# Kernel optimization log

Measured on AMD Instinct MI355X. Metric: run time of the kernel, lower is better.

The kernel has to match this reference:

```python
import jax, jax.numpy as jnp
import numpy as np

NMS_THR = 0.5
SCORE_THR = 0.05
MAX_BOXES = 300
N_ANCHORS = 5000
N_CLASSES = 80
IMG = 640.0  # image size used to scale synthetic box coords


def setup_inputs() -> dict:
    key = jax.random.key(0)
    k1, k2, k3 = jax.random.split(key, 3)
    # build well-formed boxes (x1<=x2, y1<=y2) in a 640x640 image
    c1 = jax.random.uniform(k1, (1, N_ANCHORS, 2), jnp.float32) * IMG
    c2 = jax.random.uniform(k2, (1, N_ANCHORS, 2), jnp.float32) * IMG
    boxes = jnp.concatenate([jnp.minimum(c1, c2), jnp.maximum(c1, c2) + 1.0], axis=-1)
    # classification scores in [0,1], squared to skew toward low values like sigmoid logits
    classification = jax.random.uniform(k3, (1, N_ANCHORS, N_CLASSES), jnp.float32) ** 2
    return {"boxes": boxes, "classification": classification}


def _iou_matrix(b):
    # b: [N,4] as (x1,y1,x2,y2) -> [N,N] pairwise IoU
    x1, y1, x2, y2 = b[:, 0], b[:, 1], b[:, 2], b[:, 3]
    area = (x2 - x1) * (y2 - y1)
    iw = jnp.maximum(jnp.minimum(x2[:, None], x2[None, :]) - jnp.maximum(x1[:, None], x1[None, :]), 0.0)
    ih = jnp.maximum(jnp.minimum(y2[:, None], y2[None, :]) - jnp.maximum(y1[:, None], y1[None, :]), 0.0)
    inter = iw * ih
    union = area[:, None] + area[None, :] - inter
    return inter / jnp.maximum(union, 1e-8)


def _nms_one_class(scores, iou):
    # greedy NMS for one class; scores: [N], iou: [N,N] (shared across classes)
    n = scores.shape[0]
    order = jnp.argsort(-scores)          # descending score order
    valid = scores > SCORE_THR            # per-class score-threshold filter
    idxs = jnp.arange(n)

    def step(carry, oi):
        suppressed, kept, count = carry
        alive = (~suppressed[oi]) & valid[oi] & (count < MAX_BOXES)
        # a kept box suppresses all others with IoU above threshold
        suppressed = suppressed | (alive & (iou[oi] > NMS_THR) & (idxs != oi))
        kept = kept.at[oi].set(alive)
        return (suppressed, kept, count + alive.astype(jnp.int32)), None

    init = (jnp.zeros(n, jnp.bool_), jnp.zeros(n, jnp.bool_), jnp.int32(0))
    (_, kept, _), _ = jax.lax.scan(step, init, order)
    return kept  # [N] bool mask in original index space


def reference(boxes, classification):
    b = boxes[0]             # [N,4]
    cls = classification[0]  # [N,C]
    iou = _iou_matrix(b)     # [N,N], class-independent
    kept = jax.vmap(_nms_one_class, in_axes=(1, None))(cls, iou)  # [C,N]
    # scatter surviving scores back to dense per-class score map (zeros elsewhere)
    selected = jnp.where(kept.T, cls, 0.0)                        # [N,C]
    detections = jnp.concatenate([b, selected], axis=1)           # [N,4+C]
    return detections[None]                                       # [1,N,4+C]
```

## Files before the change

### kernel.cpp

```cpp
#include <hip/hip_runtime.h>

#define N_ANCHORS 5000
#define N_CLASSES 80
#define OUT_COLS  84
#define MAX_BOXES 300
#define SCORE_THR 0.05f

#define SORT_PAD  5056
#define SIDX_PAD  5120
#define NB        4096
#define SLOTS     8
#define DONEP     0x40000000
#define NIW       3
#define NSW       4

typedef unsigned long long u64;
typedef unsigned int u32;
typedef unsigned short u16;

#define WG __HIP_MEMORY_SCOPE_WORKGROUP

__device__ __forceinline__ float readlane_f(float v, int l) {
    return __int_as_float(__builtin_amdgcn_readlane(__float_as_int(v), l));
}
__device__ __forceinline__ u64 aload64(u64* p) {
    return __hip_atomic_load(p, __ATOMIC_ACQUIRE, WG);
}
__device__ __forceinline__ int bucket_of(float s) {
    float u = sqrtf(s);
    int b = (int)((u - 0.2236f) * 5275.0f);
    return (NB - 1) - min(max(b, 0), NB - 1);
}
__device__ __forceinline__ bool iou3(float4 a, float aa, float4 q, float aq) {
    float iw = fmaxf(fminf(a.z, q.z) - fmaxf(a.x, q.x), 0.0f);
    float ih = fminf(a.w, q.w) - fmaxf(a.y, q.y);
    return 3.0f * (iw * ih) > aa + aq;
}

__global__ __launch_bounds__(1024) void nms_sort(const float* __restrict__ cls,
                                                 const float* __restrict__ boxesf,
                                                 float* __restrict__ out,
                                                 u16* __restrict__ sidx,
                                                 u32* __restrict__ totals) {
    __shared__ __align__(16) char SMEM[56896];
    u64* lk   = (u64*)SMEM;
    u32* hist = (u32*)(SMEM + 40448);
    u32* wtot = (u32*)(SMEM + 56832);

    const int c = blockIdx.x;
    const int t = threadIdx.x;
    const int lane = t & 63;
    const int wv = t >> 6;

    u32 sb[5];
    #pragma unroll
    for (int m = 0; m < 5; ++m) {
        int j = m * 1024 + t;
        float v = (j < N_ANCHORS) ? cls[(size_t)j * N_CLASSES + c] : 0.0f;
        sb[m] = (v > SCORE_THR) ? __float_as_uint(v) : 0u;
    }
    for (int i = t; i < N_ANCHORS; i += 1024)
        out[(size_t)i * OUT_COLS + 4 + c] = 0.0f;
    if (c < 4)
        for (int i = t; i < N_ANCHORS; i += 1024)
            out[(size_t)i * OUT_COLS + c] = boxesf[(size_t)i * 4 + c];

    for (int b = t; b < NB; b += 1024) hist[b] = 0u;
    __syncthreads();
    #pragma unroll
    for (int m = 0; m < 5; ++m)
        if (sb[m]) atomicAdd(&hist[bucket_of(__uint_as_float(sb[m]))], 1u);
    __syncthreads();

    const int hbase = t * 4;
    u32 vals[4]; u32 run = 0;
    #pragma unroll
    for (int k = 0; k < 4; ++k) { run += hist[hbase + k]; vals[k] = run; }
    u32 x = run;
    #pragma unroll
    for (int off = 1; off < 64; off <<= 1) { u32 y = __shfl_up(x, off); if (lane >= off) x += y; }
    if (lane == 63) wtot[wv] = x;
    __syncthreads();
    u32 woff = 0;
    for (int w = 0; w < wv; ++w) woff += wtot[w];
    const u32 exb = woff + x - run;
    #pragma unroll
    for (int k = 0; k < 4; ++k) hist[hbase + k] = exb + (k ? vals[k - 1] : 0u);
    __syncthreads();
    #pragma unroll
    for (int m = 0; m < 5; ++m) {
        if (sb[m]) {
            int j = m * 1024 + t;
            u32 pos = atomicAdd(&hist[bucket_of(__uint_as_float(sb[m]))], 1u);
            lk[pos] = ((u64)sb[m] << 32) | (u32)(~(u32)j);
        }
    }
    __syncthreads();
    const int total = (int)hist[NB - 1];
    for (int v = total + t; v < SORT_PAD; v += 1024) lk[v] = 0ull;
    for (int b = hbase; b < hbase + 4; ++b) {
        int s0 = b ? (int)hist[b - 1] : 0;
        int e  = (int)hist[b];
        for (int i = s0 + 1; i < e; ++i) {
            u64 key = lk[i]; int q = i - 1;
            while (q >= s0 && lk[q] < key) { lk[q + 1] = lk[q]; --q; }
            lk[q + 1] = key;
        }
    }
    __syncthreads();
    u16* sc_ = sidx + (size_t)c * SIDX_PAD;
    for (int v = t; v < SIDX_PAD; v += 1024) {
        u64 e = (v < SORT_PAD) ? lk[v] : 0ull;
        sc_[v] = e ? (u16)(~(u32)e) : (u16)0xFFFF;
    }
    if (t == 0) totals[c] = (u32)total;
}

__global__ __launch_bounds__(512, 1) void nms_scan(const float* __restrict__ cls,
                                                   const float4* __restrict__ boxes4,
                                                   const u16* __restrict__ sidx,
                                                   const u32* __restrict__ totals,
                                                   float* __restrict__ out) {
    __shared__ __align__(16) char SMEM[19200];
    u64*    Iring   = (u64*)SMEM;
    float4* Bring   = (float4*)(SMEM + 4096);
    float4* kbox    = (float4*)(SMEM + 12288);
    float*  karea   = (float*)(SMEM + 17152);
    u16*    kout16  = (u16*)(SMEM + 18368);
    u64*    KS      = (u64*)(SMEM + 18976);
    u32*    KBa     = (u32*)(SMEM + 19040);
    u64*    flagIK  = (u64*)(SMEM + 19072);
    u32*    flagIK32= (u32*)(SMEM + 19072);
    u64*    progcnt = (u64*)(SMEM + 19136);

    const int c = blockIdx.x;
    const int t = threadIdx.x;
    const int lane = t & 63;
    const int wv = t >> 6;
    const u16* sc_ = sidx + (size_t)c * SIDX_PAD;

    if (t < 304) { kbox[t] = make_float4(1e9f, 1e9f, 1e9f, 1e9f); karea[t] = 1e18f; }
    if (t < SLOTS) flagIK[t] = 0ull;
    if (t == 0) *progcnt = 0ull;
    __syncthreads();
    const int total = (int)totals[c];
    const int nch = (total + 63) >> 6;

    if (wv >= 1 && wv <= NIW) {
        for (int j = wv - 1; j < nch; j += NIW) {
            const int slot = j & (SLOTS - 1);
            u16 g = sc_[j * 64 + lane];
            u32 jj = (g != 0xFFFF) ? g : 0u;
            float4 bx = boxes4[jj];
            float ar = (bx.z - bx.x) * (bx.w - bx.y);
            u64 word = 0ull;
            #pragma unroll 16
            for (int q = 0; q < 64; ++q) {
                float4 o;
                o.x = readlane_f(bx.x, q); o.y = readlane_f(bx.y, q);
                o.z = readlane_f(bx.z, q); o.w = readlane_f(bx.w, q);
                float aq = readlane_f(ar, q);
                float iw = fmaxf(fminf(bx.z, o.z) - fmaxf(bx.x, o.x), 0.0f);
                float ih = fminf(bx.w, o.w) - fmaxf(bx.y, o.y);
                if (3.0f * (iw * ih) > ar + aq) word |= (1ull << q);
            }
            u32 p;
            for (;;) {
                p = (u32)aload64(progcnt);
                if ((int)p >= j - (SLOTS - 1)) break;
                __builtin_amdgcn_s_sleep(2);
            }
            if (p >= DONEP) return;
            Iring[slot * 64 + lane] = word;
            if (lane == 0)
                __hip_atomic_store(&flagIK32[slot * 2 + 1], (u32)(j + 1), __ATOMIC_RELEASE, WG);
        }
        return;
    }
    if (wv > NIW) {
        for (int j = wv - (NIW + 1); j < nch; j += NSW) {
            const int slot = j & (SLOTS - 1);
            u16 g = sc_[j * 64 + lane];
            bool validL = (g != 0xFFFF);
            u32 jj = validL ? g : 0u;
            float4 bx = boxes4[jj];
            float ar = (bx.z - bx.x) * (bx.w - bx.y);
            u64 pk;
            for (;;) {
                pk = aload64(progcnt);
                if ((int)(u32)pk >= j - (SLOTS - 1)) break;
                __builtin_amdgcn_s_sleep(2);
            }
            if ((u32)pk >= DONEP) return;
            Bring[slot * 64 + lane] = bx;
            bool sup = !validL;
            u32 done = 0; bool alldead = false;
            for (;;) {
                u32 kn = (u32)(pk >> 32);
                u32 r4 = kn & ~3u;
                for (u32 r = done; r < r4; r += 4) {
                    float4 q0 = kbox[r], q1 = kbox[r+1], q2 = kbox[r+2], q3 = kbox[r+3];
                    float4 a4 = *(const float4*)(karea + r);
                    sup = sup | iou3(bx,ar,q0,a4.x) | iou3(bx,ar,q1,a4.y)
                              | iou3(bx,ar,q2,a4.z) | iou3(bx,ar,q3,a4.w);
                    if (((r >> 2) & 7u) == 7u && !__ballot(!sup)) { alldead = true; break; }
                }
                if (alldead) break;
                for (u32 r = r4; r < kn; ++r)
                    sup = sup | iou3(bx, ar, kbox[r], karea[r]);
                done = r4;
                if ((int)(u32)pk >= j - 2) break;
                __builtin_amdgcn_s_sleep(1);
                pk = aload64(progcnt);
            }
            u64 ksf = __ballot(sup);
            if (lane == 0) {
                KS[slot] = ksf; KBa[slot] = (u32)(pk >> 32);
                __hip_atomic_store(&flagIK32[slot * 2], (u32)(j + 1), __ATOMIC_RELEASE, WG);
            }
            if ((u32)pk >= DONEP) return;
        }
        return;
    }

    __builtin_amdgcn_s_setprio(3);
    int kept = 0; u32 kcur = 0; bool capped = false;
    u16 key = (nch > 0) ? sc_[lane] : (u16)0xFFFF;
    for (int k = 0; k < nch; ++k) {
        const int slot = k & (SLOTS - 1);
        bool valid = (key != 0xFFFF);
        u32 j = valid ? key : 0u;

        const u64 want = ((u64)(u32)(k + 1) << 32) | (u32)(k + 1);
        while (aload64(&flagIK[slot]) != want) { }
        u64 ks = KS[slot];
        u32 kb = KBa[slot];
        float4 bx = Bring[slot * 64 + lane];
        u64 I = Iring[slot * 64 + lane];
        if (ks != ~0ull) {
            float ar = (bx.z - bx.x) * (bx.w - bx.y);
            bool alive = valid && !((ks >> lane) & 1ull);
            u32 r1 = (kcur + 3) & ~3u;
            for (u32 r = kb & ~3u; r < r1; r += 4) {
                float4 q0 = kbox[r], q1 = kbox[r + 1], q2 = kbox[r + 2], q3 = kbox[r + 3];
                float4 a4 = *(const float4*)(karea + r);
                bool s = iou3(bx, ar, q0, a4.x) | iou3(bx, ar, q1, a4.y)
                       | iou3(bx, ar, q2, a4.z) | iou3(bx, ar, q3, a4.w);
                alive = alive && !s;
            }
            u64 rem = __ballot(alive);
            if (rem) {
                u64 km = 0ull;
                while (rem) {
                    int pos = __ffsll((long long)rem) - 1;
                    km |= 1ull << pos;
                    if (++kept == MAX_BOXES) { capped = true; break; }
                    u32 lo = (u32)__builtin_amdgcn_readlane((int)(u32)I, pos);
                    u32 hi = (u32)__builtin_amdgcn_readlane((int)(u32)(I >> 32), pos);
                    rem &= ~(((u64)hi << 32) | (u64)lo);
                }
                if ((km >> lane) & 1ull) {
                    int rank = (int)__popcll(km & ((1ull << lane) - 1ull));
                    kbox[kcur + rank] = bx;
                    karea[kcur + rank] = ar;
                    kout16[kcur + rank] = (u16)j;
                }
                kcur += (u32)__popcll(km);
            }
        }
        if (capped) break;
        if (lane == 0)
            __hip_atomic_store(progcnt, ((u64)kcur << 32) | (u32)(k + 1),
                               __ATOMIC_RELEASE, WG);
        if (k + 1 < nch) key = sc_[(k + 1) * 64 + lane];
    }
    if (lane == 0)
        __hip_atomic_store(progcnt, ((u64)kcur << 32) | DONEP, __ATOMIC_RELEASE, WG);
    __builtin_amdgcn_s_setprio(0);

    for (u32 i = (u32)lane; i < kcur; i += 64) {
        u32 idx = kout16[i];
        out[(size_t)idx * OUT_COLS + 4 + c] = cls[(size_t)idx * N_CLASSES + c];
    }
}

extern "C" void kernel_launch(void* const* d_in, const int* in_sizes, int n_in,
                              void* d_out, int out_size, void* d_ws, size_t ws_size,
                              hipStream_t stream) {
    const float* boxes = (const float*)d_in[0];
    const float* cls   = (const float*)d_in[1];
    float* out = (float*)d_out;
    u16* sidx   = (u16*)d_ws;
    u32* totals = (u32*)((char*)d_ws + N_CLASSES * SIDX_PAD * 2);
    nms_sort<<<N_CLASSES, 1024, 0, stream>>>(cls, boxes, out, sidx, totals);
    nms_scan<<<N_CLASSES, 512, 0, stream>>>(cls, (const float4*)boxes, sidx, totals, out);
}
```

Measured before the change: 149.0 us.

## Coalesce output init, pad histogram banks, unroll IoU loop by 8, rebalance waves

Output initialization now has each class block write a contiguous chunk of 63 rows with all 84 columns, replacing the strided per-column writes. The LDS histogram index is padded (b + b/32) to reduce bank conflicts during atomics and the scan. The suppression IoU loop is unrolled from 4 to 8 kept boxes per iteration, with the early-exit ballot still every 32 boxes. The split of waves between IoU and suppression roles changes from 3/4 to 2/5. Together these target memory coalescing and LDS contention, though the padding uses more shared memory and the wave split may shift the bottleneck.

```diff
diff --git a/kernel.cpp b/kernel.cpp
--- a/kernel.cpp
+++ b/kernel.cpp
@@ -11,14 +11,15 @@
 #define NB        4096
 #define SLOTS     8
 #define DONEP     0x40000000
-#define NIW       3
-#define NSW       4
+#define NIW       2
+#define NSW       5
 
 typedef unsigned long long u64;
 typedef unsigned int u32;
 typedef unsigned short u16;
 
 #define WG __HIP_MEMORY_SCOPE_WORKGROUP
+#define HP(b) ((b) + ((b) >> 5))
 
 __device__ __forceinline__ float readlane_f(float v, int l) {
     return __int_as_float(__builtin_amdgcn_readlane(__float_as_int(v), l));
@@ -42,10 +43,10 @@
                                                  float* __restrict__ out,
                                                  u16* __restrict__ sidx,
                                                  u32* __restrict__ totals) {
-    __shared__ __align__(16) char SMEM[56896];
+    __shared__ __align__(16) char SMEM[57408];
     u64* lk   = (u64*)SMEM;
     u32* hist = (u32*)(SMEM + 40448);
-    u32* wtot = (u32*)(SMEM + 56832);
+    u32* wtot = (u32*)(SMEM + 57344);
 
     const int c = blockIdx.x;
     const int t = threadIdx.x;
@@ -59,23 +60,29 @@
         float v = (j < N_ANCHORS) ? cls[(size_t)j * N_CLASSES + c] : 0.0f;
         sb[m] = (v > SCORE_THR) ? __float_as_uint(v) : 0u;
     }
-    for (int i = t; i < N_ANCHORS; i += 1024)
-        out[(size_t)i * OUT_COLS + 4 + c] = 0.0f;
-    if (c < 4)
-        for (int i = t; i < N_ANCHORS; i += 1024)
-            out[(size_t)i * OUT_COLS + c] = boxesf[(size_t)i * 4 + c];
-
-    for (int b = t; b < NB; b += 1024) hist[b] = 0u;
+    {
+        const int r0 = c * 63;
+        const int rend = min(r0 + 63, N_ANCHORS);
+        const int nel = (rend - r0) * OUT_COLS;
+        float* ob = out + (size_t)r0 * OUT_COLS;
+        for (int i = t; i < nel; i += 1024) {
+            int row = r0 + i / OUT_COLS;
+            int col = i - (i / OUT_COLS) * OUT_COLS;
+            ob[i] = (col < 4) ? boxesf[(size_t)row * 4 + col] : 0.0f;
+        }
+    }
+
+    for (int b = t; b < HP(NB - 1) + 1; b += 1024) hist[b] = 0u;
     __syncthreads();
     #pragma unroll
     for (int m = 0; m < 5; ++m)
-        if (sb[m]) atomicAdd(&hist[bucket_of(__uint_as_float(sb[m]))], 1u);
+        if (sb[m]) atomicAdd(&hist[HP(bucket_of(__uint_as_float(sb[m])))], 1u);
     __syncthreads();
 
     const int hbase = t * 4;
     u32 vals[4]; u32 run = 0;
     #pragma unroll
-    for (int k = 0; k < 4; ++k) { run += hist[hbase + k]; vals[k] = run; }
+    for (int k = 0; k < 4; ++k) { run += hist[HP(hbase + k)]; vals[k] = run; }
     u32 x = run;
     #pragma unroll
     for (int off = 1; off < 64; off <<= 1) { u32 y = __shfl_up(x, off); if (lane >= off) x += y; }
@@ -85,22 +92,22 @@
     for (int w = 0; w < wv; ++w) woff += wtot[w];
     const u32 exb = woff + x - run;
     #pragma unroll
-    for (int k = 0; k < 4; ++k) hist[hbase + k] = exb + (k ? vals[k - 1] : 0u);
+    for (int k = 0; k < 4; ++k) hist[HP(hbase + k)] = exb + (k ? vals[k - 1] : 0u);
     __syncthreads();
     #pragma unroll
     for (int m = 0; m < 5; ++m) {
         if (sb[m]) {
             int j = m * 1024 + t;
-            u32 pos = atomicAdd(&hist[bucket_of(__uint_as_float(sb[m]))], 1u);
+            u32 pos = atomicAdd(&hist[HP(bucket_of(__uint_as_float(sb[m])))], 1u);
             lk[pos] = ((u64)sb[m] << 32) | (u32)(~(u32)j);
         }
     }
     __syncthreads();
-    const int total = (int)hist[NB - 1];
+    const int total = (int)hist[HP(NB - 1)];
     for (int v = total + t; v < SORT_PAD; v += 1024) lk[v] = 0ull;
     for (int b = hbase; b < hbase + 4; ++b) {
-        int s0 = b ? (int)hist[b - 1] : 0;
-        int e  = (int)hist[b];
+        int s0 = b ? (int)hist[HP(b - 1)] : 0;
+        int e  = (int)hist[HP(b)];
         for (int i = s0 + 1; i < e; ++i) {
             u64 key = lk[i]; int q = i - 1;
             while (q >= s0 && lk[q] < key) { lk[q + 1] = lk[q]; --q; }
@@ -197,18 +204,23 @@
             u32 done = 0; bool alldead = false;
             for (;;) {
                 u32 kn = (u32)(pk >> 32);
-                u32 r4 = kn & ~3u;
-                for (u32 r = done; r < r4; r += 4) {
-                    float4 q0 = kbox[r], q1 = kbox[r+1], q2 = kbox[r+2], q3 = kbox[r+3];
-                    float4 a4 = *(const float4*)(karea + r);
-                    sup = sup | iou3(bx,ar,q0,a4.x) | iou3(bx,ar,q1,a4.y)
-                              | iou3(bx,ar,q2,a4.z) | iou3(bx,ar,q3,a4.w);
-                    if (((r >> 2) & 7u) == 7u && !__ballot(!sup)) { alldead = true; break; }
+                u32 r8 = kn & ~7u;
+                for (u32 r = done; r < r8; r += 8) {
+                    float4 q0 = kbox[r+0], q1 = kbox[r+1], q2 = kbox[r+2], q3 = kbox[r+3];
+                    float4 q4 = kbox[r+4], q5 = kbox[r+5], q6 = kbox[r+6], q7 = kbox[r+7];
+                    float4 a40 = *(const float4*)(karea + r);
+                    float4 a41 = *(const float4*)(karea + r + 4);
+                    sup = sup | iou3(bx,ar,q0,a40.x) | iou3(bx,ar,q1,a40.y)
+                              | iou3(bx,ar,q2,a40.z) | iou3(bx,ar,q3,a40.w)
+                              | iou3(bx,ar,q4,a41.x) | iou3(bx,ar,q5,a41.y)
+                              | iou3(bx,ar,q6,a41.z) | iou3(bx,ar,q7,a41.w);
+                    if (((r >> 3) & 3u) == 3u && !__ballot(!sup)) { alldead = true; break; }
                 }
                 if (alldead) break;
-                for (u32 r = r4; r < kn; ++r)
+                u32 d2 = (r8 > done) ? r8 : done;
+                for (u32 r = d2; r < kn; ++r)
                     sup = sup | iou3(bx, ar, kbox[r], karea[r]);
-                done = r4;
+                done = d2;
                 if ((int)(u32)pk >= j - 2) break;
                 __builtin_amdgcn_s_sleep(1);
                 pk = aload64(progcnt);
```

Result: faster. 144.6 us (-2.9%).
